# Kernel optimization log

Hardware: AMD Instinct MI355X
Metric: run time of the kernel (lower is better)

The kernel has to match this reference:

```python
import jax, jax.numpy as jnp
import numpy as np

B, T, C = 8, 1024, 2048  # batch, seq_len (<= T_MAX=1024), n_embd == dim_att


def setup_inputs() -> dict:
    key = jax.random.key(0)
    ks = jax.random.split(key, 10)
    inp = {
        "x": jax.random.normal(ks[0], (B, T, C), dtype=jnp.float32),
        "time_decay": jax.random.normal(ks[1], (C,), dtype=jnp.float32),
        "time_first": jax.random.normal(ks[2], (C,), dtype=jnp.float32),
        "time_mix_k": jax.random.uniform(ks[3], (C,), dtype=jnp.float32),
        "time_mix_v": jax.random.uniform(ks[4], (C,), dtype=jnp.float32),
        "time_mix_r": jax.random.uniform(ks[5], (C,), dtype=jnp.float32),
        "Wk": jax.random.normal(ks[6], (C, C), dtype=jnp.float32) / np.sqrt(C),
        "Wv": jax.random.normal(ks[7], (C, C), dtype=jnp.float32) / np.sqrt(C),
        "Wr": jax.random.normal(ks[8], (C, C), dtype=jnp.float32) / np.sqrt(C),
        "Wo": jax.random.normal(ks[9], (C, C), dtype=jnp.float32) / np.sqrt(C),
    }
    return inp


def _wkv(time_decay, time_first, k, v):
    # Numerically-stabilized RWKV linear-attention recurrence (rwkv_linear_attention_cpu).
    # k, v: [B, T, C]; state tracked in float32.
    w = -jnp.exp(time_decay.astype(jnp.float32))  # [C]
    u = time_first.astype(jnp.float32)            # [C]
    kf = k.astype(jnp.float32)
    vf = v.astype(jnp.float32)

    def step(carry, kv):
        num, den, mx = carry           # each [B, C]
        kt, vt = kv                    # each [B, C]
        max_out = jnp.maximum(mx, kt + u)
        e1 = jnp.exp(mx - max_out)
        e2 = jnp.exp(kt + u - max_out)
        out = (e1 * num + e2 * vt) / (e1 * den + e2)
        max_st = jnp.maximum(mx + w, kt)
        e1s = jnp.exp(mx + w - max_st)
        e2s = jnp.exp(kt - max_st)
        return (e1s * num + e2s * vt, e1s * den + e2s, max_st), out

    Bn, Tn, Cn = k.shape
    init = (jnp.zeros((Bn, Cn), jnp.float32),
            jnp.zeros((Bn, Cn), jnp.float32),
            jnp.full((Bn, Cn), -1e38, jnp.float32))
    kT = jnp.swapaxes(kf, 0, 1)  # [T, B, C]
    vT = jnp.swapaxes(vf, 0, 1)
    _, outs = jax.lax.scan(step, init, (kT, vT))
    return jnp.swapaxes(outs, 0, 1).astype(k.dtype)  # [B, T, C]


def reference(x, time_decay, time_first, time_mix_k, time_mix_v, time_mix_r, Wk, Wv, Wr, Wo):
    # time_shift: shift sequence right by one, zero at t=0
    shifted = jnp.pad(x, ((0, 0), (1, 0), (0, 0)))[:, :-1]
    xk = x * time_mix_k + shifted * (1.0 - time_mix_k)
    xv = x * time_mix_v + shifted * (1.0 - time_mix_v)
    xr = x * time_mix_r + shifted * (1.0 - time_mix_r)
    k = jnp.einsum('btc,dc->btd', xk, Wk)
    v = jnp.einsum('btc,dc->btd', xv, Wv)
    r = jnp.einsum('btc,dc->btd', xr, Wr)
    sr = jax.nn.sigmoid(r)
    rwkv = _wkv(time_decay, time_first, k, v)
    return jnp.einsum('btd,cd->btc', sr * rwkv, Wo)
```

## Files before the change

### kernel.cpp

```cpp
#include <hip/hip_runtime.h>
#include <stdint.h>

#define B_DIM 8
#define T_DIM 1024
#define C_DIM 2048
#define M_DIM (B_DIM * T_DIM)
#define SEG   32
#define SEGL  (T_DIM / SEG)

typedef __bf16 bf16x8 __attribute__((ext_vector_type(8)));
typedef __bf16 bf16x4 __attribute__((ext_vector_type(4)));
typedef float  f32x4  __attribute__((ext_vector_type(4)));

__device__ __forceinline__ void gld_lds16(const void* g, void* l) {
    __builtin_amdgcn_global_load_lds((__attribute__((address_space(1))) void*)g,
                                     (__attribute__((address_space(3))) void*)l,
                                     16, 0, 0);
}

__global__ __launch_bounds__(256) void cast_w_kernel(
    const float* __restrict__ w0, const float* __restrict__ w1,
    const float* __restrict__ w2, const float* __restrict__ w3,
    __bf16* __restrict__ dst) {
    const float* srcs[4] = {w0, w1, w2, w3};
    const float* s = srcs[blockIdx.y];
    __bf16* d = dst + (size_t)blockIdx.y * (size_t)C_DIM * C_DIM;
    const size_t i = ((size_t)blockIdx.x * 256 + threadIdx.x) * 4;
    f32x4 v = *(const f32x4*)(s + i);
    bf16x4 o;
#pragma unroll
    for (int j = 0; j < 4; ++j) o[j] = (__bf16)v[j];
    *(bf16x4*)(d + i) = o;
}

__global__ __launch_bounds__(256) void mix4_kernel(
    const float* __restrict__ x,
    const float* __restrict__ mk, const float* __restrict__ mv,
    const float* __restrict__ mr,
    __bf16* __restrict__ xk, __bf16* __restrict__ xv, __bf16* __restrict__ xr) {
    const size_t idx = ((size_t)blockIdx.x * 256 + threadIdx.x) * 4;
    const int c = (int)(idx & (C_DIM - 1));
    const int t = (int)((idx >> 11) & (T_DIM - 1));

    f32x4 xc = *(const f32x4*)(x + idx);
    f32x4 sh = {0.f, 0.f, 0.f, 0.f};
    if (t != 0) sh = *(const f32x4*)(x + idx - C_DIM);
    f32x4 k4 = *(const f32x4*)(mk + c);
    f32x4 v4 = *(const f32x4*)(mv + c);
    f32x4 r4 = *(const f32x4*)(mr + c);

    bf16x4 ok, ov, orr;
#pragma unroll
    for (int j = 0; j < 4; ++j) {
        float xx = xc[j], ss = sh[j];
        ok[j]  = (__bf16)(xx * k4[j] + ss * (1.f - k4[j]));
        ov[j]  = (__bf16)(xx * v4[j] + ss * (1.f - v4[j]));
        orr[j] = (__bf16)(xx * r4[j] + ss * (1.f - r4[j]));
    }
    *(bf16x4*)(xk + idx) = ok;
    *(bf16x4*)(xv + idx) = ov;
    *(bf16x4*)(xr + idx) = orr;
}

template <bool OUTF32>
__global__ __launch_bounds__(256) void gemm_bt(
    const __bf16* __restrict__ A, const __bf16* __restrict__ W,
    void* __restrict__ Cout, int M, int N, int K) {
    __shared__ __align__(16) __bf16 As[128 * 64];
    __shared__ __align__(16) __bf16 Bs[128 * 64];

    const int tid  = threadIdx.x;
    const int lane = tid & 63;
    const int wave = tid >> 6;
    const int row0 = blockIdx.x * 128;
    const int col0 = blockIdx.y * 128;
    const int wm = (wave & 1) * 64;
    const int wn = (wave >> 1) * 64;

    f32x4 acc[4][4] = {};

    const int sr = tid >> 3;
    const int sc = ((tid & 7) ^ (sr & 7)) * 8;
    const __bf16* Ap = A + (size_t)(row0 + sr) * K + sc;
    const __bf16* Bp = W + (size_t)(col0 + sr) * K + sc;
    __bf16* AsW = As + wave * 512;
    __bf16* BsW = Bs + wave * 512;

    const int mrow = lane & 15;
    const int q    = lane >> 4;

    for (int k0 = 0; k0 < K; k0 += 64) {
        __syncthreads();
#pragma unroll
        for (int j = 0; j < 4; ++j) {
            gld_lds16(Ap + k0 + (size_t)(32 * j) * K, AsW + 2048 * j);
            gld_lds16(Bp + k0 + (size_t)(32 * j) * K, BsW + 2048 * j);
        }
        __syncthreads();

#pragma unroll
        for (int kk = 0; kk < 2; ++kk) {
            const int swz = ((q + 4 * kk) ^ (mrow & 7)) * 8;
            bf16x8 af[4], bfr[4];
#pragma unroll
            for (int i = 0; i < 4; ++i)
                af[i]  = *(const bf16x8*)(As + (size_t)(wm + mrow + i * 16) * 64 + swz);
#pragma unroll
            for (int i = 0; i < 4; ++i)
                bfr[i] = *(const bf16x8*)(Bs + (size_t)(wn + mrow + i * 16) * 64 + swz);
#pragma unroll
            for (int im = 0; im < 4; ++im)
#pragma unroll
                for (int in = 0; in < 4; ++in)
                    acc[im][in] = __builtin_amdgcn_mfma_f32_16x16x32_bf16(
                        af[im], bfr[in], acc[im][in], 0, 0, 0);
        }
    }

    const int crow = (lane >> 4) * 4;
    const int ccol = lane & 15;
#pragma unroll
    for (int im = 0; im < 4; ++im)
#pragma unroll
        for (int in = 0; in < 4; ++in)
#pragma unroll
            for (int r = 0; r < 4; ++r) {
                int row = row0 + wm + im * 16 + crow + r;
                int col = col0 + wn + in * 16 + ccol;
                if constexpr (OUTF32) {
                    ((float*)Cout)[(size_t)row * N + col] = acc[im][in][r];
                } else {
                    ((__bf16*)Cout)[(size_t)row * N + col] = (__bf16)acc[im][in][r];
                }
            }
}

__global__ __launch_bounds__(256) void wkv_pass1(
    const __bf16* __restrict__ kbuf, const __bf16* __restrict__ vbuf,
    const float* __restrict__ td,
    float* __restrict__ st_num, float* __restrict__ st_den,
    float* __restrict__ st_m) {
    const int c = blockIdx.x * 256 + threadIdx.x;
    const int b = blockIdx.y;
    const int s = blockIdx.z;
    const size_t base = (size_t)b * T_DIM * C_DIM + (size_t)s * SEGL * C_DIM + c;

    const float w = -__expf(td[c]);
    float num = 0.f, den = 0.f, mx = -1e38f;

    for (int t0 = 0; t0 < SEGL; t0 += 8) {
        float kt[8], vt[8];
#pragma unroll
        for (int j = 0; j < 8; ++j) {
            const size_t idx = base + (size_t)(t0 + j) * C_DIM;
            kt[j] = (float)kbuf[idx];
            vt[j] = (float)vbuf[idx];
        }
#pragma unroll
        for (int j = 0; j < 8; ++j) {
            float ms  = fmaxf(mx + w, kt[j]);
            float e1s = __expf(mx + w - ms);
            float e2s = __expf(kt[j] - ms);
            num = e1s * num + e2s * vt[j];
            den = e1s * den + e2s;
            mx  = ms;
        }
    }
    const size_t sidx = (size_t)s * (B_DIM * C_DIM) + (size_t)b * C_DIM + c;
    st_num[sidx] = num;
    st_den[sidx] = den;
    st_m[sidx]   = mx;
}

__global__ __launch_bounds__(256) void wkv_pass2(
    const float* __restrict__ td,
    float* __restrict__ st_num, float* __restrict__ st_den,
    float* __restrict__ st_m) {
    const int bc = blockIdx.x * 256 + threadIdx.x;
    const int c  = bc & (C_DIM - 1);
    const float w = -__expf(td[c]);
    const float wL = w * SEGL;

    float num = 0.f, den = 0.f, mx = -1e38f;
    for (int s = 0; s < SEG; ++s) {
        const size_t sidx = (size_t)s * (B_DIM * C_DIM) + bc;
        float na = st_num[sidx], da = st_den[sidx], ma = st_m[sidx];
        st_num[sidx] = num; st_den[sidx] = den; st_m[sidx] = mx;
        float md = mx + wL;
        float mc = fmaxf(md, ma);
        float e1 = __expf(md - mc);
        float e2 = __expf(ma - mc);
        num = e1 * num + e2 * na;
        den = e1 * den + e2 * da;
        mx  = mc;
    }
}

__global__ __launch_bounds__(256) void wkv_pass3(
    const __bf16* __restrict__ kbuf, const __bf16* __restrict__ vbuf,
    const __bf16* __restrict__ rbuf, const float* __restrict__ td,
    const float* __restrict__ tf,
    const float* __restrict__ st_num, const float* __restrict__ st_den,
    const float* __restrict__ st_m, __bf16* __restrict__ abuf) {
    const int c = blockIdx.x * 256 + threadIdx.x;
    const int b = blockIdx.y;
    const int s = blockIdx.z;
    const size_t base = (size_t)b * T_DIM * C_DIM + (size_t)s * SEGL * C_DIM + c;

    const float w = -__expf(td[c]);
    const float u = tf[c];
    const size_t sidx = (size_t)s * (B_DIM * C_DIM) + (size_t)b * C_DIM + c;
    float num = st_num[sidx], den = st_den[sidx], mx = st_m[sidx];

    for (int t0 = 0; t0 < SEGL; t0 += 8) {
        float kt[8], vt[8], rt[8];
#pragma unroll
        for (int j = 0; j < 8; ++j) {
            const size_t idx = base + (size_t)(t0 + j) * C_DIM;
            kt[j] = (float)kbuf[idx];
            vt[j] = (float)vbuf[idx];
            rt[j] = (float)rbuf[idx];
        }
#pragma unroll
        for (int j = 0; j < 8; ++j) {
            float mo  = fmaxf(mx, kt[j] + u);
            float e1  = __expf(mx - mo);
            float e2  = __expf(kt[j] + u - mo);
            float out = (e1 * num + e2 * vt[j]) / (e1 * den + e2);

            float ms  = fmaxf(mx + w, kt[j]);
            float e1s = __expf(mx + w - ms);
            float e2s = __expf(kt[j] - ms);
            num = e1s * num + e2s * vt[j];
            den = e1s * den + e2s;
            mx  = ms;

            float sr = 1.f / (1.f + __expf(-rt[j]));
            abuf[base + (size_t)(t0 + j) * C_DIM] = (__bf16)(sr * out);
        }
    }
}

extern "C" void kernel_launch(void* const* d_in, const int* in_sizes, int n_in,
                              void* d_out, int out_size, void* d_ws, size_t ws_size,
                              hipStream_t stream) {
    (void)in_sizes; (void)n_in; (void)out_size; (void)ws_size;
    const float* x  = (const float*)d_in[0];
    const float* td = (const float*)d_in[1];
    const float* tf = (const float*)d_in[2];
    const float* mk = (const float*)d_in[3];
    const float* mv = (const float*)d_in[4];
    const float* mr = (const float*)d_in[5];
    const float* Wk = (const float*)d_in[6];
    const float* Wv = (const float*)d_in[7];
    const float* Wr = (const float*)d_in[8];
    const float* Wo = (const float*)d_in[9];
    float* out = (float*)d_out;

    const size_t WN = (size_t)C_DIM * C_DIM;
    const size_t n  = (size_t)M_DIM * C_DIM;

    __bf16* Wb  = (__bf16*)d_ws;
    __bf16* Wkb = Wb;
    __bf16* Wvb = Wb + WN;
    __bf16* Wrb = Wb + 2 * WN;
    __bf16* Wob = Wb + 3 * WN;
    __bf16* xk  = Wb + 4 * WN;
    __bf16* xv  = xk + n;
    __bf16* xr  = xv + n;
    __bf16* kb  = xr + n;
    __bf16* vb  = xk;
    __bf16* rb  = xv;
    __bf16* ab  = xr;

    float* st_num = (float*)d_ws;
    float* st_den = st_num + (size_t)SEG * B_DIM * C_DIM;
    float* st_m   = st_den + (size_t)SEG * B_DIM * C_DIM;

    cast_w_kernel<<<dim3((unsigned)(WN / 4 / 256), 4), 256, 0, stream>>>(
        Wk, Wv, Wr, Wo, Wb);

    mix4_kernel<<<dim3((unsigned)(n / 4 / 256)), 256, 0, stream>>>(
        x, mk, mv, mr, xk, xv, xr);

    dim3 ggrid(M_DIM / 128, C_DIM / 128);
    gemm_bt<false><<<ggrid, 256, 0, stream>>>(xk, Wkb, kb, M_DIM, C_DIM, C_DIM);
    gemm_bt<false><<<ggrid, 256, 0, stream>>>(xv, Wvb, vb, M_DIM, C_DIM, C_DIM);
    gemm_bt<false><<<ggrid, 256, 0, stream>>>(xr, Wrb, rb, M_DIM, C_DIM, C_DIM);

    dim3 wgrid(C_DIM / 256, B_DIM, SEG);
    wkv_pass1<<<wgrid, 256, 0, stream>>>(kb, vb, td, st_num, st_den, st_m);
    wkv_pass2<<<dim3(B_DIM * C_DIM / 256), 256, 0, stream>>>(
        td, st_num, st_den, st_m);
    wkv_pass3<<<wgrid, 256, 0, stream>>>(kb, vb, rb, td, tf,
                                         st_num, st_den, st_m, ab);

    gemm_bt<true><<<ggrid, 256, 0, stream>>>(ab, Wob, out, M_DIM, C_DIM, C_DIM);
}
```

Measured before the change: 585.2 us.

## Replace GEMM with 256x256-tile, 4-stage pipelined 8-wave MFMA kernel

Replaces the 128x128 single-buffered GEMM with a 256x256 tile kernel using 8 waves, a 4-deep LDS ring of 32-wide K slices loaded via global_load_lds, manual vmcnt/lgkmcnt waits, interleaved barriers and setprio around MFMA bursts. It also remaps block IDs for grouped L2 reuse. The aim is to hide global load latency behind MFMA work and raise arithmetic intensity per loaded byte. In exchange it uses 128 KB of LDS per block and many accumulator registers, and the hand-tuned waits and barriers are fragile.

```diff
diff --git a/kernel.cpp b/kernel.cpp
--- a/kernel.cpp
+++ b/kernel.cpp
@@ -62,75 +62,129 @@
     *(bf16x4*)(xr + idx) = orr;
 }
 
+#define VMCNT(N) asm volatile("s_waitcnt vmcnt(" #N ")" ::: "memory")
+#define LGKM0()  do { asm volatile("s_waitcnt lgkmcnt(0)" ::: "memory"); \
+                      __builtin_amdgcn_sched_barrier(0); } while (0)
+
+#define MFMA4(mi, a)                                                              \
+    acc[mi][0] = __builtin_amdgcn_mfma_f32_16x16x32_bf16(a, b0, acc[mi][0], 0, 0, 0); \
+    acc[mi][1] = __builtin_amdgcn_mfma_f32_16x16x32_bf16(a, b1, acc[mi][1], 0, 0, 0); \
+    acc[mi][2] = __builtin_amdgcn_mfma_f32_16x16x32_bf16(a, b2, acc[mi][2], 0, 0, 0); \
+    acc[mi][3] = __builtin_amdgcn_mfma_f32_16x16x32_bf16(a, b3, acc[mi][3], 0, 0, 0)
+
+#define STAGE_A(TT, NB)                                                           \
+    do { const __bf16* g_ = Ag + (TT) * 32;                                       \
+         __bf16* l_ = lA + (NB) * 8192;                                           \
+         gld_lds16(g_, l_);                                                       \
+         gld_lds16(g_ + (size_t)128 * C_DIM, l_ + 4096); } while (0)
+
+#define STAGE_B(TT, NB)                                                           \
+    do { const __bf16* g_ = Bg + (TT) * 32;                                       \
+         __bf16* l_ = lB + (NB) * 8192;                                           \
+         gld_lds16(g_, l_);                                                       \
+         gld_lds16(g_ + (size_t)128 * C_DIM, l_ + 4096); } while (0)
+
+#define GBLOCK(BUF, DO_STAGE, TT, DO_VM, VM)                                      \
+  { const char* pa = fA + (BUF) * 16384;                                          \
+    const char* pb = fB + (BUF) * 16384;                                          \
+    bf16x8 af0 = *(const bf16x8*)(pa);                                            \
+    bf16x8 af1 = *(const bf16x8*)(pa + 1024);                                     \
+    bf16x8 af2 = *(const bf16x8*)(pa + 2048);                                     \
+    bf16x8 af3 = *(const bf16x8*)(pa + 3072);                                     \
+    bf16x8 b0  = *(const bf16x8*)(pb);                                            \
+    bf16x8 b1  = *(const bf16x8*)(pb + 1024);                                     \
+    bf16x8 b2  = *(const bf16x8*)(pb + 2048);                                     \
+    bf16x8 b3  = *(const bf16x8*)(pb + 3072);                                     \
+    if (DO_STAGE) { STAGE_A(TT, ((BUF) + 3) & 3); }                               \
+    __builtin_amdgcn_s_barrier();                                                 \
+    LGKM0();                                                                      \
+    __builtin_amdgcn_s_setprio(1);                                                \
+    MFMA4(0, af0); MFMA4(1, af1); MFMA4(2, af2); MFMA4(3, af3);                   \
+    __builtin_amdgcn_s_setprio(0);                                                \
+    __builtin_amdgcn_s_barrier();                                                 \
+    af0 = *(const bf16x8*)(pa + 4096);                                            \
+    af1 = *(const bf16x8*)(pa + 5120);                                            \
+    af2 = *(const bf16x8*)(pa + 6144);                                            \
+    af3 = *(const bf16x8*)(pa + 7168);                                            \
+    if (DO_STAGE) { STAGE_B(TT, ((BUF) + 3) & 3); }                               \
+    __builtin_amdgcn_s_barrier();                                                 \
+    LGKM0();                                                                      \
+    __builtin_amdgcn_s_setprio(1);                                                \
+    MFMA4(4, af0); MFMA4(5, af1); MFMA4(6, af2); MFMA4(7, af3);                   \
+    __builtin_amdgcn_s_setprio(0);                                                \
+    if (DO_VM) { VMCNT(VM); }                                                     \
+    __builtin_amdgcn_s_barrier();                                                 \
+  }
+
 template <bool OUTF32>
-__global__ __launch_bounds__(256) void gemm_bt(
+__global__ __launch_bounds__(512, 2) void gemm256_bt(
     const __bf16* __restrict__ A, const __bf16* __restrict__ W,
-    void* __restrict__ Cout, int M, int N, int K) {
-    __shared__ __align__(16) __bf16 As[128 * 64];
-    __shared__ __align__(16) __bf16 Bs[128 * 64];
+    void* __restrict__ Cout) {
+    __shared__ __align__(16) __bf16 sA[4 * 8192];
+    __shared__ __align__(16) __bf16 sB[4 * 8192];
 
     const int tid  = threadIdx.x;
     const int lane = tid & 63;
     const int wave = tid >> 6;
-    const int row0 = blockIdx.x * 128;
-    const int col0 = blockIdx.y * 128;
-    const int wm = (wave & 1) * 64;
-    const int wn = (wave >> 1) * 64;
-
-    f32x4 acc[4][4] = {};
-
-    const int sr = tid >> 3;
-    const int sc = ((tid & 7) ^ (sr & 7)) * 8;
-    const __bf16* Ap = A + (size_t)(row0 + sr) * K + sc;
-    const __bf16* Bp = W + (size_t)(col0 + sr) * K + sc;
-    __bf16* AsW = As + wave * 512;
-    __bf16* BsW = Bs + wave * 512;
-
-    const int mrow = lane & 15;
-    const int q    = lane >> 4;
-
-    for (int k0 = 0; k0 < K; k0 += 64) {
-        __syncthreads();
-#pragma unroll
-        for (int j = 0; j < 4; ++j) {
-            gld_lds16(Ap + k0 + (size_t)(32 * j) * K, AsW + 2048 * j);
-            gld_lds16(Bp + k0 + (size_t)(32 * j) * K, BsW + 2048 * j);
-        }
-        __syncthreads();
-
-#pragma unroll
-        for (int kk = 0; kk < 2; ++kk) {
-            const int swz = ((q + 4 * kk) ^ (mrow & 7)) * 8;
-            bf16x8 af[4], bfr[4];
-#pragma unroll
-            for (int i = 0; i < 4; ++i)
-                af[i]  = *(const bf16x8*)(As + (size_t)(wm + mrow + i * 16) * 64 + swz);
-#pragma unroll
-            for (int i = 0; i < 4; ++i)
-                bfr[i] = *(const bf16x8*)(Bs + (size_t)(wn + mrow + i * 16) * 64 + swz);
-#pragma unroll
-            for (int im = 0; im < 4; ++im)
-#pragma unroll
-                for (int in = 0; in < 4; ++in)
-                    acc[im][in] = __builtin_amdgcn_mfma_f32_16x16x32_bf16(
-                        af[im], bfr[in], acc[im][in], 0, 0, 0);
-        }
-    }
+    const int wr   = wave >> 2;
+    const int wc   = wave & 3;
+
+    const int bid = blockIdx.x;
+    const int wid = (bid & 7) * 32 + (bid >> 3);
+    const int m_blk = wid & 31;
+    const int n_blk = wid >> 5;
+    const int row0 = m_blk * 256;
+    const int col0 = n_blk * 256;
+
+    const int u  = tid >> 3;
+    const int z  = (tid & 7) ^ (u & 7);
+    const int srow = 2 * u + (z >> 2);
+    const int scol = (z & 3) * 8;
+    const __bf16* Ag = A + (size_t)(row0 + srow) * C_DIM + scol;
+    const __bf16* Bg = W + (size_t)(col0 + srow) * C_DIM + scol;
+    __bf16* lA = sA + wave * 512;
+    __bf16* lB = sB + wave * 512;
+
+    const int l15 = lane & 15, l2 = l15 >> 1;
+    const int lbyte = l2 * 128 + ((((lane >> 4) + ((lane & 1) << 2)) ^ l2) << 4);
+    const char* fA = (const char*)sA + wr * 8192 + lbyte;
+    const char* fB = (const char*)sB + wc * 4096 + lbyte;
+
+    f32x4 acc[8][4] = {};
+
+    const int NT = C_DIM / 32;
+
+    STAGE_A(0, 0); STAGE_B(0, 0);
+    STAGE_A(1, 1); STAGE_B(1, 1);
+    STAGE_A(2, 2); STAGE_B(2, 2);
+    VMCNT(8);
+    __builtin_amdgcn_s_barrier();
+
+#pragma unroll 1
+    for (int t = 0; t < NT - 4; t += 4) {
+        GBLOCK(0, true, t + 3, true, 8);
+        GBLOCK(1, true, t + 4, true, 8);
+        GBLOCK(2, true, t + 5, true, 8);
+        GBLOCK(3, true, t + 6, true, 8);
+    }
+    GBLOCK(0, true,  NT - 1, true, 8);
+    GBLOCK(1, false, 0,      true, 4);
+    GBLOCK(2, false, 0,      true, 0);
+    GBLOCK(3, false, 0,      false, 0);
 
     const int crow = (lane >> 4) * 4;
-    const int ccol = lane & 15;
-#pragma unroll
-    for (int im = 0; im < 4; ++im)
-#pragma unroll
-        for (int in = 0; in < 4; ++in)
+#pragma unroll
+    for (int mf = 0; mf < 8; ++mf)
+#pragma unroll
+        for (int jf = 0; jf < 4; ++jf)
 #pragma unroll
             for (int r = 0; r < 4; ++r) {
-                int row = row0 + wm + im * 16 + crow + r;
-                int col = col0 + wn + in * 16 + ccol;
+                const int row = row0 + wr * 128 + mf * 16 + crow + r;
+                const int col = col0 + wc * 64 + jf * 16 + l15;
                 if constexpr (OUTF32) {
-                    ((float*)Cout)[(size_t)row * N + col] = acc[im][in][r];
+                    ((float*)Cout)[(size_t)row * C_DIM + col] = acc[mf][jf][r];
                 } else {
-                    ((__bf16*)Cout)[(size_t)row * N + col] = (__bf16)acc[im][in][r];
+                    ((__bf16*)Cout)[(size_t)row * C_DIM + col] = (__bf16)acc[mf][jf][r];
                 }
             }
 }
@@ -283,10 +337,10 @@
     mix4_kernel<<<dim3((unsigned)(n / 4 / 256)), 256, 0, stream>>>(
         x, mk, mv, mr, xk, xv, xr);
 
-    dim3 ggrid(M_DIM / 128, C_DIM / 128);
-    gemm_bt<false><<<ggrid, 256, 0, stream>>>(xk, Wkb, kb, M_DIM, C_DIM, C_DIM);
-    gemm_bt<false><<<ggrid, 256, 0, stream>>>(xv, Wvb, vb, M_DIM, C_DIM, C_DIM);
-    gemm_bt<false><<<ggrid, 256, 0, stream>>>(xr, Wrb, rb, M_DIM, C_DIM, C_DIM);
+    dim3 ggrid((M_DIM / 256) * (C_DIM / 256));
+    gemm256_bt<false><<<ggrid, 512, 0, stream>>>(xk, Wkb, kb);
+    gemm256_bt<false><<<ggrid, 512, 0, stream>>>(xv, Wvb, vb);
+    gemm256_bt<false><<<ggrid, 512, 0, stream>>>(xr, Wrb, rb);
 
     dim3 wgrid(C_DIM / 256, B_DIM, SEG);
     wkv_pass1<<<wgrid, 256, 0, stream>>>(kb, vb, td, st_num, st_den, st_m);
@@ -295,5 +349,5 @@
     wkv_pass3<<<wgrid, 256, 0, stream>>>(kb, vb, rb, td, tf,
                                          st_num, st_den, st_m, ab);
 
-    gemm_bt<true><<<ggrid, 256, 0, stream>>>(ab, Wob, out, M_DIM, C_DIM, C_DIM);
-}
+    gemm256_bt<true><<<ggrid, 512, 0, stream>>>(ab, Wob, out);
+}
```

Result: faster. 530.3 us (-9.4%).

## Replace GEMM with 256x256 double-buffered, software-pipelined 8-wave kernel

Applied to the files above, without the earlier changes.

Replaces the 128x128 single-buffered GEMM with a 256x256-tile kernel using 512 threads, double-buffered LDS, and manual waitcnt/sched_barrier interleaving, so global-to-LDS loads for the next K step overlap with MFMA work. It also adds an XCD-aware block-index remap to improve L2 locality, and sets MFMA priority around compute bursts. The larger tile raises arithmetic intensity per byte loaded. The cost is 128 KB of LDS per block and heavy register pressure from 32 accumulators. The kernel also hardcodes the problem dimensions.

```diff
diff --git a/kernel.cpp b/kernel.cpp
--- a/kernel.cpp
+++ b/kernel.cpp
@@ -62,75 +62,160 @@
     *(bf16x4*)(xr + idx) = orr;
 }
 
+#define LGKM(N)  do { asm volatile("s_waitcnt lgkmcnt(" #N ")" ::: "memory"); \
+                      __builtin_amdgcn_sched_barrier(0); } while (0)
+#define VM0()    asm volatile("s_waitcnt vmcnt(0)" ::: "memory")
+
+#define MF1(mi, jj, AV, BV) \
+    acc[mi][jj] = __builtin_amdgcn_mfma_f32_16x16x32_bf16(AV, BV, acc[mi][jj], 0, 0, 0)
+
+#define MFMA16(MB, AA, BB)                                                        \
+    __builtin_amdgcn_s_setprio(1);                                                \
+    MF1(MB+0,0,AA[0],BB[0]); MF1(MB+0,1,AA[0],BB[1]);                             \
+    MF1(MB+0,2,AA[0],BB[2]); MF1(MB+0,3,AA[0],BB[3]);                             \
+    MF1(MB+1,0,AA[1],BB[0]); MF1(MB+1,1,AA[1],BB[1]);                             \
+    MF1(MB+1,2,AA[1],BB[2]); MF1(MB+1,3,AA[1],BB[3]);                             \
+    MF1(MB+2,0,AA[2],BB[0]); MF1(MB+2,1,AA[2],BB[1]);                             \
+    MF1(MB+2,2,AA[2],BB[2]); MF1(MB+2,3,AA[2],BB[3]);                             \
+    MF1(MB+3,0,AA[3],BB[0]); MF1(MB+3,1,AA[3],BB[1]);                             \
+    MF1(MB+3,2,AA[3],BB[2]); MF1(MB+3,3,AA[3],BB[3]);                             \
+    __builtin_amdgcn_s_setprio(0)
+
+#define STAGE8(KOF, BOE)                                                          \
+    do {                                                                          \
+        gld_lds16(Ag + (KOF),                       lA + (BOE));                  \
+        gld_lds16(Bg + (KOF),                       lB + (BOE));                  \
+        gld_lds16(Ag + (KOF) + (size_t)64*C_DIM,    lA + (BOE) + 4096);           \
+        gld_lds16(Bg + (KOF) + (size_t)64*C_DIM,    lB + (BOE) + 4096);           \
+        gld_lds16(Ag + (KOF) + (size_t)128*C_DIM,   lA + (BOE) + 8192);           \
+        gld_lds16(Bg + (KOF) + (size_t)128*C_DIM,   lB + (BOE) + 8192);           \
+        gld_lds16(Ag + (KOF) + (size_t)192*C_DIM,   lA + (BOE) + 12288);          \
+        gld_lds16(Bg + (KOF) + (size_t)192*C_DIM,   lB + (BOE) + 12288);          \
+    } while (0)
+
 template <bool OUTF32>
-__global__ __launch_bounds__(256) void gemm_bt(
+__global__ __launch_bounds__(512, 2) void gemm256_bt(
     const __bf16* __restrict__ A, const __bf16* __restrict__ W,
-    void* __restrict__ Cout, int M, int N, int K) {
-    __shared__ __align__(16) __bf16 As[128 * 64];
-    __shared__ __align__(16) __bf16 Bs[128 * 64];
+    void* __restrict__ Cout) {
+    __shared__ __align__(16) __bf16 sA[2 * 16384];
+    __shared__ __align__(16) __bf16 sB[2 * 16384];
 
     const int tid  = threadIdx.x;
     const int lane = tid & 63;
     const int wave = tid >> 6;
-    const int row0 = blockIdx.x * 128;
-    const int col0 = blockIdx.y * 128;
-    const int wm = (wave & 1) * 64;
-    const int wn = (wave >> 1) * 64;
-
-    f32x4 acc[4][4] = {};
-
-    const int sr = tid >> 3;
-    const int sc = ((tid & 7) ^ (sr & 7)) * 8;
-    const __bf16* Ap = A + (size_t)(row0 + sr) * K + sc;
-    const __bf16* Bp = W + (size_t)(col0 + sr) * K + sc;
-    __bf16* AsW = As + wave * 512;
-    __bf16* BsW = Bs + wave * 512;
-
-    const int mrow = lane & 15;
-    const int q    = lane >> 4;
-
-    for (int k0 = 0; k0 < K; k0 += 64) {
-        __syncthreads();
-#pragma unroll
-        for (int j = 0; j < 4; ++j) {
-            gld_lds16(Ap + k0 + (size_t)(32 * j) * K, AsW + 2048 * j);
-            gld_lds16(Bp + k0 + (size_t)(32 * j) * K, BsW + 2048 * j);
-        }
-        __syncthreads();
-
-#pragma unroll
-        for (int kk = 0; kk < 2; ++kk) {
-            const int swz = ((q + 4 * kk) ^ (mrow & 7)) * 8;
-            bf16x8 af[4], bfr[4];
-#pragma unroll
-            for (int i = 0; i < 4; ++i)
-                af[i]  = *(const bf16x8*)(As + (size_t)(wm + mrow + i * 16) * 64 + swz);
-#pragma unroll
-            for (int i = 0; i < 4; ++i)
-                bfr[i] = *(const bf16x8*)(Bs + (size_t)(wn + mrow + i * 16) * 64 + swz);
-#pragma unroll
-            for (int im = 0; im < 4; ++im)
-#pragma unroll
-                for (int in = 0; in < 4; ++in)
-                    acc[im][in] = __builtin_amdgcn_mfma_f32_16x16x32_bf16(
-                        af[im], bfr[in], acc[im][in], 0, 0, 0);
-        }
+    const int wr   = wave >> 2;
+    const int wc   = wave & 3;
+
+    const int bid = blockIdx.x;
+    const int wid = (bid & 7) * 32 + (bid >> 3);
+    const int m_blk = wid & 31;
+    const int n_blk = wid >> 5;
+    const int row0 = m_blk * 256;
+    const int col0 = n_blk * 256;
+
+    const int srow = tid >> 3;
+    const int sg   = (tid & 7) ^ (srow & 7);
+    const __bf16* Ag = A + (size_t)(row0 + srow) * C_DIM + sg * 8;
+    const __bf16* Bg = W + (size_t)(col0 + srow) * C_DIM + sg * 8;
+    __bf16* lA = sA + wave * 512;
+    __bf16* lB = sB + wave * 512;
+
+    const int l15 = lane & 15;
+    const int q   = lane >> 4;
+    const int sw0 = (q ^ (l15 & 7)) * 8;
+    const int aE0 = wr * 8192 + l15 * 64 + sw0;
+    const int aE1 = aE0 ^ 32;
+    const int bE0 = wc * 4096 + l15 * 64 + sw0;
+    const int bE1 = bE0 ^ 32;
+
+    f32x4  acc[8][4] = {};
+    bf16x8 a0[4], a1[4], b0f[4], b1f[4];
+
+    STAGE8(0, 0);
+    VM0();
+    __builtin_amdgcn_s_barrier();
+#pragma unroll
+    for (int i = 0; i < 4; ++i) a0[i]  = *(const bf16x8*)(sA + aE0 + i * 1024);
+#pragma unroll
+    for (int j = 0; j < 4; ++j) b0f[j] = *(const bf16x8*)(sB + bE0 + j * 1024);
+
+#pragma unroll 1
+    for (int s = 0; s < 31; ++s) {
+        const int boe  = (s & 1) << 14;
+        const int boe1 = boe ^ 16384;
+
+#pragma unroll
+        for (int i = 0; i < 4; ++i)
+            a1[i] = *(const bf16x8*)(sA + boe + aE0 + 4096 + i * 1024);
+        STAGE8((s + 1) * 64, boe1);
+        LGKM(4);
+        MFMA16(0, a0, b0f);
+
+#pragma unroll
+        for (int i = 0; i < 4; ++i)
+            a0[i]  = *(const bf16x8*)(sA + boe + aE1 + i * 1024);
+#pragma unroll
+        for (int j = 0; j < 4; ++j)
+            b1f[j] = *(const bf16x8*)(sB + boe + bE1 + j * 1024);
+        LGKM(8);
+        MFMA16(4, a1, b0f);
+
+#pragma unroll
+        for (int i = 0; i < 4; ++i)
+            a1[i] = *(const bf16x8*)(sA + boe + aE1 + 4096 + i * 1024);
+        VM0();
+        LGKM(4);
+        MFMA16(0, a0, b1f);
+        __builtin_amdgcn_s_barrier();
+
+#pragma unroll
+        for (int i = 0; i < 4; ++i)
+            a0[i]  = *(const bf16x8*)(sA + boe1 + aE0 + i * 1024);
+#pragma unroll
+        for (int j = 0; j < 4; ++j)
+            b0f[j] = *(const bf16x8*)(sB + boe1 + bE0 + j * 1024);
+        LGKM(8);
+        MFMA16(4, a1, b1f);
+        __builtin_amdgcn_s_barrier();
+    }
+
+    {
+        const int boe = 16384;
+#pragma unroll
+        for (int i = 0; i < 4; ++i)
+            a1[i] = *(const bf16x8*)(sA + boe + aE0 + 4096 + i * 1024);
+        LGKM(4);
+        MFMA16(0, a0, b0f);
+#pragma unroll
+        for (int i = 0; i < 4; ++i)
+            a0[i]  = *(const bf16x8*)(sA + boe + aE1 + i * 1024);
+#pragma unroll
+        for (int j = 0; j < 4; ++j)
+            b1f[j] = *(const bf16x8*)(sB + boe + bE1 + j * 1024);
+        LGKM(8);
+        MFMA16(4, a1, b0f);
+#pragma unroll
+        for (int i = 0; i < 4; ++i)
+            a1[i] = *(const bf16x8*)(sA + boe + aE1 + 4096 + i * 1024);
+        LGKM(4);
+        MFMA16(0, a0, b1f);
+        LGKM(0);
+        MFMA16(4, a1, b1f);
     }
 
     const int crow = (lane >> 4) * 4;
-    const int ccol = lane & 15;
-#pragma unroll
-    for (int im = 0; im < 4; ++im)
-#pragma unroll
-        for (int in = 0; in < 4; ++in)
+#pragma unroll
+    for (int mf = 0; mf < 8; ++mf)
+#pragma unroll
+        for (int jf = 0; jf < 4; ++jf)
 #pragma unroll
             for (int r = 0; r < 4; ++r) {
-                int row = row0 + wm + im * 16 + crow + r;
-                int col = col0 + wn + in * 16 + ccol;
+                const int row = row0 + wr * 128 + mf * 16 + crow + r;
+                const int col = col0 + wc * 64 + jf * 16 + l15;
                 if constexpr (OUTF32) {
-                    ((float*)Cout)[(size_t)row * N + col] = acc[im][in][r];
+                    ((float*)Cout)[(size_t)row * C_DIM + col] = acc[mf][jf][r];
                 } else {
-                    ((__bf16*)Cout)[(size_t)row * N + col] = (__bf16)acc[im][in][r];
+                    ((__bf16*)Cout)[(size_t)row * C_DIM + col] = (__bf16)acc[mf][jf][r];
                 }
             }
 }
@@ -283,10 +368,10 @@
     mix4_kernel<<<dim3((unsigned)(n / 4 / 256)), 256, 0, stream>>>(
         x, mk, mv, mr, xk, xv, xr);
 
-    dim3 ggrid(M_DIM / 128, C_DIM / 128);
-    gemm_bt<false><<<ggrid, 256, 0, stream>>>(xk, Wkb, kb, M_DIM, C_DIM, C_DIM);
-    gemm_bt<false><<<ggrid, 256, 0, stream>>>(xv, Wvb, vb, M_DIM, C_DIM, C_DIM);
-    gemm_bt<false><<<ggrid, 256, 0, stream>>>(xr, Wrb, rb, M_DIM, C_DIM, C_DIM);
+    dim3 ggrid((M_DIM / 256) * (C_DIM / 256));
+    gemm256_bt<false><<<ggrid, 512, 0, stream>>>(xk, Wkb, kb);
+    gemm256_bt<false><<<ggrid, 512, 0, stream>>>(xv, Wvb, vb);
+    gemm256_bt<false><<<ggrid, 512, 0, stream>>>(xr, Wrb, rb);
 
     dim3 wgrid(C_DIM / 256, B_DIM, SEG);
     wkv_pass1<<<wgrid, 256, 0, stream>>>(kb, vb, td, st_num, st_den, st_m);
@@ -295,5 +380,5 @@
     wkv_pass3<<<wgrid, 256, 0, stream>>>(kb, vb, rb, td, tf,
                                          st_num, st_den, st_m, ab);
 
-    gemm_bt<true><<<ggrid, 256, 0, stream>>>(ab, Wob, out, M_DIM, C_DIM, C_DIM);
-}
+    gemm256_bt<true><<<ggrid, 512, 0, stream>>>(ab, Wob, out);
+}
```

Measured after the change: 514.7 us. -12.1%, faster.
